# Performance work log

Measured on AMD Instinct MI355X. Metric: run time of the kernel, lower is better.

## Reference

```python
import jax, jax.numpy as jnp
import numpy as np

N_PROP, N_GRID, N_KEY, C_FEAT = 128, 216, 4096, 128
RADII = (0.8, 1.6)
NSAMPLES = (16, 16)
C_OUT = 64  # per-branch MLP output channels


def setup_inputs() -> dict:
    key = jax.random.key(0)
    ks = jax.random.split(key, 20)
    s = 0.05
    return {
        "wlh": jax.random.uniform(ks[0], (N_PROP, 3)) * 4.0 + 0.5,
        "center": jax.random.normal(ks[1], (N_PROP, 3)) * 5.0,
        "yaw": jax.random.uniform(ks[2], (N_PROP,)) * 2.0 * np.pi,
        "u": jax.random.uniform(ks[3], (N_PROP, N_GRID, 3)),
        "keypoints_xyz": jax.random.normal(ks[4], (1, N_KEY, 3)) * 5.0,
        "keypoints_features": jax.random.normal(ks[5], (1, C_FEAT, N_KEY)),
        "pn0_w1": jax.random.normal(ks[6], (C_OUT, C_FEAT + 3)) * s,
        "pn0_g1": jnp.ones((C_OUT,)), "pn0_b1": jnp.zeros((C_OUT,)),
        "pn0_w2": jax.random.normal(ks[7], (C_OUT, C_OUT)) * s,
        "pn0_g2": jnp.ones((C_OUT,)), "pn0_b2": jnp.zeros((C_OUT,)),
        "pn1_w1": jax.random.normal(ks[8], (C_OUT, C_FEAT + 3)) * s,
        "pn1_g1": jnp.ones((C_OUT,)), "pn1_b1": jnp.zeros((C_OUT,)),
        "pn1_w2": jax.random.normal(ks[9], (C_OUT, C_OUT)) * s,
        "pn1_g2": jnp.ones((C_OUT,)), "pn1_b2": jnp.zeros((C_OUT,)),
        "red_w1": jax.random.normal(ks[10], (256, N_GRID * 2 * C_OUT)) * 0.01,
        "red_b1": jnp.zeros((256,)),
        "red_w2": jax.random.normal(ks[11], (256, 256)) * s,
        "red_b2": jnp.zeros((256,)),
    }


def reference(wlh, center, yaw, u, keypoints_xyz, keypoints_features,
              pn0_w1, pn0_g1, pn0_b1, pn0_w2, pn0_g2, pn0_b2,
              pn1_w1, pn1_g1, pn1_b1, pn1_w2, pn1_g2, pn1_b2,
              red_w1, red_b1, red_w2, red_b2):
    n, m, _ = u.shape
    # --- sample gridpoints inside proposals and rotate by yaw around z ---
    gp = u * wlh[:, None, :]                                 # (n, m, 3)
    c, s = jnp.cos(yaw), jnp.sin(yaw)
    R = jnp.stack([c, -s, s, c], axis=-1).reshape(-1, 2, 2)   # (n, 2, 2)
    xy = jnp.einsum('njk,nmk->nmj', R, gp[..., :2])
    grid = jnp.concatenate([xy, gp[..., 2:]], -1) + center[:, None, :]
    grid = grid.reshape(-1, 3)                               # (G, 3), G = n*m

    kp = keypoints_xyz[0]                                    # (K, 3)
    kf = jnp.transpose(keypoints_features[0])                # (K, C)
    K = kp.shape[0]

    # squared distances (G, K) without materializing (G, K, 3)
    d2 = (jnp.sum(grid * grid, -1)[:, None]
          + jnp.sum(kp * kp, -1)[None, :]
          - 2.0 * grid @ kp.T)

    def ball_query(radius, nsample):
        # first `nsample` in-radius indices in original order; pad with first
        # hit; all-zeros if no point in radius (pointnet2 CUDA semantics).
        mask = d2 < radius * radius
        cand = jnp.where(mask, jnp.arange(K, dtype=jnp.int32), K)
        srt = jnp.sort(cand, axis=-1)[:, :nsample]           # (G, ns)
        first = srt[:, :1]
        return jnp.where(srt < K, srt, jnp.where(first < K, first, 0))

    def branch(radius, nsample, w1, g1, b1, w2, g2, b2):
        idx = ball_query(radius, nsample)                    # (G, ns)
        xyz = kp[idx] - grid[:, None, :]                     # (G, ns, 3)
        x = jnp.concatenate([xyz, kf[idx]], -1)              # (G, ns, 3+C)
        h = jax.nn.relu(jnp.einsum('gnc,oc->gno', x, w1) * g1 + b1)
        h = jax.nn.relu(jnp.einsum('gnc,oc->gno', h, w2) * g2 + b2)
        return jnp.max(h, axis=1)                            # (G, C_OUT)

    f0 = branch(RADII[0], NSAMPLES[0], pn0_w1, pn0_g1, pn0_b1, pn0_w2, pn0_g2, pn0_b2)
    f1 = branch(RADII[1], NSAMPLES[1], pn1_w1, pn1_g1, pn1_b1, pn1_w2, pn1_g2, pn1_b2)
    pooled = jnp.concatenate([f0, f1], -1)                   # (G, 2*C_OUT)
    Cp = pooled.shape[-1]

    # faithful replication of (1,C,n,m).permute(0,3,1,2).view(1,n,-1)
    t = pooled.reshape(n, m, Cp)                             # gridpoint order (n, m)
    red_in = jnp.transpose(t, (1, 2, 0)).reshape(1, n, m * Cp)

    h = jax.nn.relu(red_in @ red_w1.T + red_b1)
    return jax.nn.relu(h @ red_w2.T + red_b2)                # (1, n, 256)
```

## Files before the change

### kernel.cpp

```cpp
#include <hip/hip_runtime.h>
#include <hip/hip_bf16.h>

typedef unsigned short u16;
typedef unsigned int   u32;
typedef unsigned long long u64;

#define N_PROPC 128
#define N_GRIDC 216
#define G_TOT   27648
#define N_KEYC  4096
#define C_FEATC 128
#define R0SQ    0.64f
#define R1SQ    2.56f
#define BF16_ONES_DWORD 0x3F803F80u

typedef __attribute__((ext_vector_type(8))) short bf16x8;
typedef __attribute__((ext_vector_type(4))) float f32x4;

#if __has_builtin(__builtin_amdgcn_fcmpf)
#define BALLOT_LT(a, b) __builtin_amdgcn_fcmpf((a), (b), 4)
#else
#define BALLOT_LT(a, b) __ballot((a) < (b))
#endif

__device__ __forceinline__ float bf2f(u16 u) {
    return __uint_as_float(((u32)u) << 16);
}
__device__ __forceinline__ u16 f2bf(float f) {
    u32 u = __float_as_uint(f);
    u32 r = (u + 0x7fffu + ((u >> 16) & 1u)) >> 16;
    return (u16)r;
}
__device__ __forceinline__ bool is_bf16(const u32* flagp) {
    return *flagp == BF16_ONES_DWORD;
}
__device__ __forceinline__ float ld(const void* p, int i, bool bf) {
    return bf ? bf2f(((const u16*)p)[i]) : ((const float*)p)[i];
}
__device__ __forceinline__ u16 ldb(const void* p, int i, bool bf) {
    return bf ? ((const u16*)p)[i] : f2bf(((const float*)p)[i]);
}

__global__ __launch_bounds__(256) void prep_fused_kernel(
    const u32* __restrict__ flagp,
    const void* __restrict__ kxyz,
    const void* __restrict__ wlh, const void* __restrict__ center,
    const void* __restrict__ yaw, const void* __restrict__ uu,
    const void* __restrict__ kf,
    const void* __restrict__ w10, const void* __restrict__ g10, const void* __restrict__ b10,
    const void* __restrict__ w20, const void* __restrict__ g20, const void* __restrict__ b20,
    const void* __restrict__ w11, const void* __restrict__ g11, const void* __restrict__ b11,
    const void* __restrict__ w21, const void* __restrict__ g21, const void* __restrict__ b21,
    const void* __restrict__ rw2,
    float4* __restrict__ kp4, float4* __restrict__ grid4, u16* __restrict__ kfT,
    u16* __restrict__ w1mf, u16* __restrict__ w2mf,
    float* __restrict__ g1f, float* __restrict__ b1f,
    float* __restrict__ g2f, float* __restrict__ b2f,
    float* __restrict__ w2rT)
{
    __shared__ u16 tile[64][130];
    const bool bf = is_bf16(flagp);
    const int bid = blockIdx.x, tid = threadIdx.x;

    if (bid < 16) {
        int k = bid * 256 + tid;
        float x = ld(kxyz, k*3, bf), y = ld(kxyz, k*3+1, bf), z = ld(kxyz, k*3+2, bf);
        kp4[k] = make_float4(x, y, z, 0.0f);
    } else if (bid < 124) {
        int g = (bid - 16) * 256 + tid;
        int n = g / N_GRIDC;
        float ux = ld(uu, g*3, bf), uy = ld(uu, g*3+1, bf), uz = ld(uu, g*3+2, bf);
        float gpx = ux * ld(wlh, n*3, bf);
        float gpy = uy * ld(wlh, n*3+1, bf);
        float gpz = uz * ld(wlh, n*3+2, bf);
        float yv = ld(yaw, n, bf);
        float c = cosf(yv), sn = sinf(yv);
        float x = (c*gpx - sn*gpy) + ld(center, n*3, bf);
        float y = (sn*gpx + c*gpy) + ld(center, n*3+1, bf);
        float z = gpz + ld(center, n*3+2, bf);
        grid4[g] = make_float4(x, y, z, 0.0f);
    } else if (bid < 188) {
        const int key0 = (bid - 124) * 64;
        #pragma unroll 4
        for (int rep = 0; rep < 32; ++rep) {
            int t = rep*256 + tid;
            int feat = t >> 6;
            int klo = t & 63;
            tile[klo][feat] = ldb(kf, feat * N_KEYC + key0 + klo, bf);
        }
        __syncthreads();
        #pragma unroll 4
        for (int rep = 0; rep < 32; ++rep) {
            int t = rep*256 + tid;
            int klo = t >> 7;
            int feat = t & 127;
            kfT[(key0 + klo)*128 + feat] = tile[klo][feat];
        }
    } else if (bid < 190) {
        const int b = bid - 188;
        const void* w1 = b ? w11 : w10; const void* g1v = b ? g11 : g10;
        const void* w2 = b ? w21 : w20; const void* g2v = b ? g21 : g20;
        const void* b1v = b ? b11 : b10; const void* b2v = b ? b21 : b20;
        for (int f = tid; f < 10240; f += 256) {
            int j = f & 7, t1 = f >> 3;
            int n = t1 & 15, t2 = t1 >> 4;
            int quad = t2 & 3, t3 = t2 >> 2;
            int kt = t3 % 5, nt = t3 / 5;
            int k = kt*32 + quad*8 + j;
            int o = nt*16 + n;
            u16 v = 0;
            if (k < 128)      v = ldb(w1, o*131 + 3 + k, bf);
            else if (k < 131) v = ldb(w1, o*131 + (k - 128), bf);
            w1mf[b*10240 + f] = v;
        }
        for (int f = tid; f < 4096; f += 256) {
            int j = f & 7, t1 = f >> 3;
            int n = t1 & 15, t2 = t1 >> 4;
            int quad = t2 & 3, t3 = t2 >> 2;
            int kt = t3 & 1, nt = t3 >> 1;
            int k = kt*32 + quad*8 + j;
            int o = nt*16 + n;
            w2mf[b*4096 + f] = ldb(w2, o*64 + k, bf);
        }
        if (tid < 64) {
            g1f[b*64 + tid] = ld(g1v, tid, bf);
            b1f[b*64 + tid] = ld(b1v, tid, bf);
            g2f[b*64 + tid] = ld(g2v, tid, bf);
            b2f[b*64 + tid] = ld(b2v, tid, bf);
        }
    } else {
        int t = (bid - 190) * 256 + tid;
        int o = t & 255, c = t >> 8;
        w2rT[c*256 + o] = ld(rw2, o*256 + c, bf);
    }
}

__global__ __launch_bounds__(256) void ballquery_kernel(
    const float4* __restrict__ kp4,
    const float4* __restrict__ grid4, u16* __restrict__ idx01)
{
    __shared__ __attribute__((aligned(16))) float4 sk[2048];
    const int tid = threadIdx.x;
    const int lane = tid & 63;
    const int wid = tid >> 6;
    const int g0 = blockIdx.x * 16 + wid * 4;
    const float4 gra = grid4[g0];
    const float4 grb = grid4[g0 + 1];
    const float4 grc = grid4[g0 + 2];
    const float4 grd = grid4[g0 + 3];

    u64 m0[4] = {0, 0, 0, 0};
    u64 m1[4] = {0, 0, 0, 0};
    #pragma unroll 1
    for (int pass = 0; pass < 2; ++pass) {
        if (pass) __syncthreads();
        for (int t = tid; t < 2048; t += 256) sk[t] = kp4[pass*2048 + t];
        __syncthreads();
        #pragma unroll
        for (int it = 0; it < 32; ++it) {
            const float4 kv = sk[it*64 + lane];
            const int chunk = pass*32 + it;
            float dx, dy, dz, d;
            dx = kv.x - gra.x; dy = kv.y - gra.y; dz = kv.z - gra.z;
            d = fmaf(dx, dx, fmaf(dy, dy, dz * dz));
            const u64 a1 = BALLOT_LT(d, R1SQ); const u64 a0 = BALLOT_LT(d, R0SQ);
            dx = kv.x - grb.x; dy = kv.y - grb.y; dz = kv.z - grb.z;
            d = fmaf(dx, dx, fmaf(dy, dy, dz * dz));
            const u64 b1m = BALLOT_LT(d, R1SQ); const u64 b0m = BALLOT_LT(d, R0SQ);
            dx = kv.x - grc.x; dy = kv.y - grc.y; dz = kv.z - grc.z;
            d = fmaf(dx, dx, fmaf(dy, dy, dz * dz));
            const u64 c1m = BALLOT_LT(d, R1SQ); const u64 c0m = BALLOT_LT(d, R0SQ);
            dx = kv.x - grd.x; dy = kv.y - grd.y; dz = kv.z - grd.z;
            d = fmaf(dx, dx, fmaf(dy, dy, dz * dz));
            const u64 d1m = BALLOT_LT(d, R1SQ); const u64 d0m = BALLOT_LT(d, R0SQ);
            if (lane == chunk) {
                m1[0] = a1; m0[0] = a0;
                m1[1] = b1m; m0[1] = b0m;
                m1[2] = c1m; m0[2] = c0m;
                m1[3] = d1m; m0[3] = d0m;
            }
        }
    }

    #pragma unroll
    for (int gg = 0; gg < 4; ++gg) {
        const int g = g0 + gg;
        u16* o0 = idx01 + (size_t)g * 16;
        u16* o1 = idx01 + (size_t)G_TOT * 16 + (size_t)g * 16;
        #pragma unroll
        for (int rad = 0; rad < 2; ++rad) {
            u64 mask = rad ? m1[gg] : m0[gg];
            u16* op = rad ? o1 : o0;
            const int cnt = __popcll(mask);
            int inc = cnt;
            #pragma unroll
            for (int d = 1; d < 64; d <<= 1) {
                int t = __shfl_up(inc, d);
                if (lane >= d) inc += t;
            }
            const int pre = inc - cnt;
            int firstk = (cnt > 0 && pre == 0) ? (lane*64 + __ffsll(mask) - 1) : 0x7FFFFFFF;
            #pragma unroll
            for (int d = 32; d >= 1; d >>= 1)
                firstk = min(firstk, __shfl_xor(firstk, d));
            const int total = __shfl(inc, 63);
            u64 mrem = mask;
            int p = pre;
            while (mrem != 0 && p < 16) {
                int j = __ffsll(mrem) - 1;
                op[p] = (u16)(lane*64 + j);
                mrem &= mrem - 1;
                ++p;
            }
            if (lane < 16 && lane >= total)
                op[lane] = (u16)(firstk == 0x7FFFFFFF ? 0 : firstk);
        }
    }
}

__global__ __launch_bounds__(256) void pointnet_mfma_kernel(
    const float4* __restrict__ grid4, const float4* __restrict__ kp4,
    const u16* __restrict__ kfT,
    const u16* __restrict__ w1mf, const u16* __restrict__ w2mf,
    const float* __restrict__ g1f, const float* __restrict__ b1f,
    const float* __restrict__ g2f, const float* __restrict__ b2f,
    const u16* __restrict__ idx01, u16* __restrict__ ATb)
{
    __shared__ __attribute__((aligned(16))) u16 w1s[10240];
    __shared__ __attribute__((aligned(16))) u16 w2s[4096];
    __shared__ __attribute__((aligned(16))) u16 h1s[4][32*72];
    const int tid = threadIdx.x;
    const int branch = blockIdx.y;

    {
        const uint4* s1 = (const uint4*)(w1mf + branch*10240);
        uint4* d1 = (uint4*)w1s;
        for (int t = tid; t < 1280; t += 256) d1[t] = s1[t];
        const uint4* s2 = (const uint4*)(w2mf + branch*4096);
        uint4* d2 = (uint4*)w2s;
        for (int t = tid; t < 512; t += 256) d2[t] = s2[t];
    }
    __syncthreads();

    const int wid = tid >> 6, lane = tid & 63;
    const int n = lane & 15, quad = lane >> 4;
    const int mi = blockIdx.x % N_GRIDC;
    const int nig = blockIdx.x / N_GRIDC;
    const int ni0 = nig*16 + wid*4;

    float g1v[4], b1v[4], g2v[4], b2v[4];
    #pragma unroll
    for (int nt = 0; nt < 4; ++nt) {
        g1v[nt] = g1f[branch*64 + nt*16 + n];
        b1v[nt] = b1f[branch*64 + nt*16 + n];
        g2v[nt] = g2f[branch*64 + nt*16 + n];
        b2v[nt] = b2f[branch*64 + nt*16 + n];
    }

    int idxv[4];
    #pragma unroll
    for (int gg = 0; gg < 4; ++gg) {
        const int g = (ni0 + gg) * N_GRIDC + mi;
        idxv[gg] = idx01[(size_t)branch*(G_TOT*16) + g*16 + n] & (N_KEYC - 1);
    }

    u16* __restrict__ h1w = &h1s[wid][0];

    #pragma unroll 1
    for (int p = 0; p < 2; ++p) {
        const int niA = ni0 + 2*p, niB = niA + 1;
        const int idxA = idxv[2*p], idxB = idxv[2*p + 1];
        const float4 kpA = kp4[idxA];
        const float4 kpB = kp4[idxB];
        const float4 grA = grid4[niA * N_GRIDC + mi];
        const float4 grB = grid4[niB * N_GRIDC + mi];

        const u16* __restrict__ arowA = kfT + idxA * C_FEATC;
        const u16* __restrict__ arowB = kfT + idxB * C_FEATC;
        uint4 arA[4], arB[4];
        #pragma unroll
        for (int kt = 0; kt < 4; ++kt) {
            arA[kt] = *(const uint4*)(arowA + kt*32 + quad*8);
            arB[kt] = *(const uint4*)(arowB + kt*32 + quad*8);
        }

        bf16x8 axyzA = (bf16x8)(short)0, axyzB = (bf16x8)(short)0;
        if (quad == 0) {
            axyzA[0] = (short)f2bf(kpA.x - grA.x);
            axyzA[1] = (short)f2bf(kpA.y - grA.y);
            axyzA[2] = (short)f2bf(kpA.z - grA.z);
            axyzB[0] = (short)f2bf(kpB.x - grB.x);
            axyzB[1] = (short)f2bf(kpB.y - grB.y);
            axyzB[2] = (short)f2bf(kpB.z - grB.z);
        }

        f32x4 accA[4], accB[4];
        #pragma unroll
        for (int nt = 0; nt < 4; ++nt) {
            accA[nt] = (f32x4){0.f, 0.f, 0.f, 0.f};
            accB[nt] = (f32x4){0.f, 0.f, 0.f, 0.f};
        }

        #pragma unroll
        for (int kt = 0; kt < 4; ++kt) {
            bf16x8 aA, aB;
            __builtin_memcpy(&aA, &arA[kt], 16);
            __builtin_memcpy(&aB, &arB[kt], 16);
            #pragma unroll
            for (int nt = 0; nt < 4; ++nt) {
                bf16x8 b = *(const bf16x8*)&w1s[(((nt*5 + kt)*4 + quad)*16 + n)*8];
                accA[nt] = __builtin_amdgcn_mfma_f32_16x16x32_bf16(aA, b, accA[nt], 0, 0, 0);
                accB[nt] = __builtin_amdgcn_mfma_f32_16x16x32_bf16(aB, b, accB[nt], 0, 0, 0);
            }
        }
        #pragma unroll
        for (int nt = 0; nt < 4; ++nt) {
            bf16x8 b = *(const bf16x8*)&w1s[(((nt*5 + 4)*4 + quad)*16 + n)*8];
            accA[nt] = __builtin_amdgcn_mfma_f32_16x16x32_bf16(axyzA, b, accA[nt], 0, 0, 0);
            accB[nt] = __builtin_amdgcn_mfma_f32_16x16x32_bf16(axyzB, b, accB[nt], 0, 0, 0);
        }

        #pragma unroll
        for (int nt = 0; nt < 4; ++nt) {
            #pragma unroll
            for (int r = 0; r < 4; ++r) {
                float vA = fmaxf(fmaf(accA[nt][r], g1v[nt], b1v[nt]), 0.0f);
                float vB = fmaxf(fmaf(accB[nt][r], g1v[nt], b1v[nt]), 0.0f);
                h1w[(quad*4 + r)*72 + nt*16 + n] = f2bf(vA);
                h1w[(16 + quad*4 + r)*72 + nt*16 + n] = f2bf(vB);
            }
        }

        f32x4 cA[4], cB[4];
        #pragma unroll
        for (int nt = 0; nt < 4; ++nt) {
            cA[nt] = (f32x4){0.f, 0.f, 0.f, 0.f};
            cB[nt] = (f32x4){0.f, 0.f, 0.f, 0.f};
        }
        #pragma unroll
        for (int kt = 0; kt < 2; ++kt) {
            bf16x8 a2A = *(const bf16x8*)&h1w[n*72 + kt*32 + quad*8];
            bf16x8 a2B = *(const bf16x8*)&h1w[(16 + n)*72 + kt*32 + quad*8];
            #pragma unroll
            for (int nt = 0; nt < 4; ++nt) {
                bf16x8 b = *(const bf16x8*)&w2s[(((nt*2 + kt)*4 + quad)*16 + n)*8];
                cA[nt] = __builtin_amdgcn_mfma_f32_16x16x32_bf16(a2A, b, cA[nt], 0, 0, 0);
                cB[nt] = __builtin_amdgcn_mfma_f32_16x16x32_bf16(a2B, b, cB[nt], 0, 0, 0);
            }
        }

        #pragma unroll
        for (int nt = 0; nt < 4; ++nt) {
            float vA = fmaxf(fmaxf(fmaxf(fmaf(cA[nt][0], g2v[nt], b2v[nt]), 0.0f),
                                   fmaxf(fmaf(cA[nt][1], g2v[nt], b2v[nt]), 0.0f)),
                             fmaxf(fmaxf(fmaf(cA[nt][2], g2v[nt], b2v[nt]), 0.0f),
                                   fmaxf(fmaf(cA[nt][3], g2v[nt], b2v[nt]), 0.0f)));
            float vB = fmaxf(fmaxf(fmaxf(fmaf(cB[nt][0], g2v[nt], b2v[nt]), 0.0f),
                                   fmaxf(fmaf(cB[nt][1], g2v[nt], b2v[nt]), 0.0f)),
                             fmaxf(fmaxf(fmaf(cB[nt][2], g2v[nt], b2v[nt]), 0.0f),
                                   fmaxf(fmaf(cB[nt][3], g2v[nt], b2v[nt]), 0.0f)));
            vA = fmaxf(vA, __shfl_xor(vA, 16));
            vA = fmaxf(vA, __shfl_xor(vA, 32));
            vB = fmaxf(vB, __shfl_xor(vB, 16));
            vB = fmaxf(vB, __shfl_xor(vB, 32));
            if (lane < 16) {
                const int ci = branch*64 + nt*16 + n;
                ATb[mi*16384 + ci*128 + niA] = f2bf(vA);
                ATb[mi*16384 + ci*128 + niB] = f2bf(vB);
            }
        }
    }
}

__global__ __launch_bounds__(256) void red1_mfma_kernel(
    const u32* __restrict__ flagp,
    const u16* __restrict__ ATb, const void* __restrict__ rw1,
    float* __restrict__ part)
{
    const bool bf = is_bf16(flagp);
    const int tid = threadIdx.x;
    const int wid = tid >> 6, lane = tid & 63;
    const int b = blockIdx.x;
    const int kc = b & 15;
    const int nt = (b >> 4) & 15;
    const int mt = (b >> 8) * 4 + wid;
    const int n = lane & 15, quad = lane >> 4;
    const int o = nt*16 + n;

    const u16* __restrict__ arow = ATb + (size_t)(mt*16 + n) * 27648;

    f32x4 acc = {0.f, 0.f, 0.f, 0.f};
    if (bf) {
        const u16* __restrict__ brow = (const u16*)rw1 + (size_t)o * 27648;
        #pragma unroll 2
        for (int s = 0; s < 54; ++s) {
            const int kk = kc*54 + s;
            uint4 araw = *(const uint4*)(arow + kk*32 + quad*8);
            bf16x8 a;
            __builtin_memcpy(&a, &araw, 16);
            uint4 braw = *(const uint4*)(brow + kk*32 + quad*8);
            bf16x8 bb;
            __builtin_memcpy(&bb, &braw, 16);
            acc = __builtin_amdgcn_mfma_f32_16x16x32_bf16(a, bb, acc, 0, 0, 0);
        }
    } else {
        const float* __restrict__ brow = (const float*)rw1 + (size_t)o * 27648;
        #pragma unroll 2
        for (int s = 0; s < 54; ++s) {
            const int kk = kc*54 + s;
            uint4 araw = *(const uint4*)(arow + kk*32 + quad*8);
            bf16x8 a;
            __builtin_memcpy(&a, &araw, 16);
            const float4 f0 = *(const float4*)(brow + kk*32 + quad*8);
            const float4 f1 = *(const float4*)(brow + kk*32 + quad*8 + 4);
            bf16x8 bb;
            bb[0] = (short)f2bf(f0.x); bb[1] = (short)f2bf(f0.y);
            bb[2] = (short)f2bf(f0.z); bb[3] = (short)f2bf(f0.w);
            bb[4] = (short)f2bf(f1.x); bb[5] = (short)f2bf(f1.y);
            bb[6] = (short)f2bf(f1.z); bb[7] = (short)f2bf(f1.w);
            acc = __builtin_amdgcn_mfma_f32_16x16x32_bf16(a, bb, acc, 0, 0, 0);
        }
    }
    #pragma unroll
    for (int r = 0; r < 4; ++r) {
        const int i = mt*16 + quad*4 + r;
        part[kc*32768 + i*256 + nt*16 + n] = acc[r];
    }
}

__global__ __launch_bounds__(256) void tail_kernel(
    const u32* __restrict__ flagp,
    const float* __restrict__ part, const void* __restrict__ rb1,
    const float* __restrict__ w2rT, const void* __restrict__ rb2,
    void* __restrict__ outp)
{
    __shared__ float hs[256];
    const bool bf = is_bf16(flagp);
    const int o = threadIdx.x, i = blockIdx.x;
    float s = ld(rb1, o, bf);
    #pragma unroll
    for (int kc = 0; kc < 16; ++kc) s += part[kc*32768 + i*256 + o];
    hs[o] = fmaxf(s, 0.0f);
    __syncthreads();
    float s2 = ld(rb2, o, bf);
    #pragma unroll 8
    for (int c = 0; c < 256; ++c)
        s2 = fmaf(hs[c], w2rT[c*256 + o], s2);
    float v = fmaxf(s2, 0.0f);
    if (bf) ((u16*)outp)[i*256 + o] = f2bf(v);
    else    ((float*)outp)[i*256 + o] = v;
}


extern "C" void kernel_launch(void* const* d_in, const int* in_sizes, int n_in,
                              void* d_out, int out_size, void* d_ws, size_t ws_size,
                              hipStream_t stream) {
    const void* wlh    = d_in[0];
    const void* center = d_in[1];
    const void* yaw    = d_in[2];
    const void* uu     = d_in[3];
    const void* kxyz   = d_in[4];
    const void* kfeat  = d_in[5];
    const void* p0w1 = d_in[6];  const void* p0g1 = d_in[7];
    const void* p0b1 = d_in[8];  const void* p0w2 = d_in[9];
    const void* p0g2 = d_in[10]; const void* p0b2 = d_in[11];
    const void* p1w1 = d_in[12]; const void* p1g1 = d_in[13];
    const void* p1b1 = d_in[14]; const void* p1w2 = d_in[15];
    const void* p1g2 = d_in[16]; const void* p1b2 = d_in[17];
    const void* rw1 = d_in[18];
    const void* rb1 = d_in[19];
    const void* rw2 = d_in[20];
    const void* rb2 = d_in[21];
    const u32* flagp = (const u32*)d_in[7];

    char* w = (char*)d_ws;
    float4* kp4   = (float4*)(w + 65536);
    float4* grid4 = (float4*)(w + 131072);
    u16*    kfT   = (u16*)(w + 573440);
    u16*    w1mf  = (u16*)(w + 1622016);
    u16*    w2mf  = (u16*)(w + 1662976);
    float*  g1f   = (float*)(w + 1679360);
    float*  b1f   = (float*)(w + 1679872);
    float*  g2f   = (float*)(w + 1680384);
    float*  b2f   = (float*)(w + 1680896);
    float*  w2rT  = (float*)(w + 1721856);
    u16*    idx01 = (u16*)(w + 1984000);
    u16*    ATb   = (u16*)(w + 3754496);
    float*  part  = (float*)(w + 32066048);

    prep_fused_kernel<<<446, 256, 0, stream>>>(flagp,
        kxyz, wlh, center, yaw, uu, kfeat,
        p0w1, p0g1, p0b1, p0w2, p0g2, p0b2,
        p1w1, p1g1, p1b1, p1w2, p1g2, p1b2,
        rw2,
        kp4, grid4, kfT,
        w1mf, w2mf, g1f, b1f, g2f, b2f, w2rT);

    ballquery_kernel<<<G_TOT/16, 256, 0, stream>>>(kp4, grid4, idx01);

    dim3 pngrid(G_TOT/16, 2);
    pointnet_mfma_kernel<<<pngrid, 256, 0, stream>>>(grid4, kp4, kfT, w1mf, w2mf,
                                                     g1f, b1f, g2f, b2f, idx01, ATb);

    red1_mfma_kernel<<<512, 256, 0, stream>>>(flagp, ATb, rw1, part);
    tail_kernel<<<128, 256, 0, stream>>>(flagp, part, rb1, w2rT, rb2, d_out);
}
```

Baseline: 271.7 us.

## Pre-convert reduce weights to bf16 in prep, double split-K, serialize pointnet halves

Adds a prep stage that converts the large red_w1 matrix (256 x 27648) to packed bf16 in workspace, so the red1 GEMM always takes the bf16 path and drops its runtime flag branch. The red1 split-K factor goes from 16 to 32, doubling the block count, and tail_kernel sums 32 partial slices. In the pointnet kernel the two gridpoints of each pair are now processed one after the other, halving the h1 shared buffer and packing the two bf16 outputs into a single 32-bit store. For fp32 inputs the conversion reads the full fp32 weight once and writes a bf16 copy, which adds traffic and about 14k extra prep blocks, and the extra partial slices cost more writes and reads.

Result: faster. 260.9 us (-4.0%).

```diff
diff --git a/kernel.cpp b/kernel.cpp
--- a/kernel.cpp
+++ b/kernel.cpp
@@ -51,12 +51,12 @@
     const void* __restrict__ w20, const void* __restrict__ g20, const void* __restrict__ b20,
     const void* __restrict__ w11, const void* __restrict__ g11, const void* __restrict__ b11,
     const void* __restrict__ w21, const void* __restrict__ g21, const void* __restrict__ b21,
-    const void* __restrict__ rw2,
+    const void* __restrict__ rw2, const void* __restrict__ rw1,
     float4* __restrict__ kp4, float4* __restrict__ grid4, u16* __restrict__ kfT,
     u16* __restrict__ w1mf, u16* __restrict__ w2mf,
     float* __restrict__ g1f, float* __restrict__ b1f,
     float* __restrict__ g2f, float* __restrict__ b2f,
-    float* __restrict__ w2rT)
+    float* __restrict__ w2rT, u32* __restrict__ rw1bf)
 {
     __shared__ u16 tile[64][130];
     const bool bf = is_bf16(flagp);
@@ -128,10 +128,19 @@
             g2f[b*64 + tid] = ld(g2v, tid, bf);
             b2f[b*64 + tid] = ld(b2v, tid, bf);
         }
-    } else {
+    } else if (bid < 446) {
         int t = (bid - 190) * 256 + tid;
         int o = t & 255, c = t >> 8;
         w2rT[c*256 + o] = ld(rw2, o*256 + c, bf);
+    } else {
+        int t = (bid - 446) * 256 + tid;
+        if (bf) {
+            rw1bf[t] = ((const u32*)rw1)[t];
+        } else {
+            const float* s = (const float*)rw1;
+            u32 lo = f2bf(s[2*t]), hi = f2bf(s[2*t + 1]);
+            rw1bf[t] = lo | (hi << 16);
+        }
     }
 }
 
@@ -228,7 +237,7 @@
 {
     __shared__ __attribute__((aligned(16))) u16 w1s[10240];
     __shared__ __attribute__((aligned(16))) u16 w2s[4096];
-    __shared__ __attribute__((aligned(16))) u16 h1s[4][32*72];
+    __shared__ __attribute__((aligned(16))) u16 h1s[4][16*72];
     const int tid = threadIdx.x;
     const int branch = blockIdx.y;
 
@@ -268,12 +277,12 @@
 
     #pragma unroll 1
     for (int p = 0; p < 2; ++p) {
-        const int niA = ni0 + 2*p, niB = niA + 1;
+        const int niA = ni0 + 2*p;
         const int idxA = idxv[2*p], idxB = idxv[2*p + 1];
         const float4 kpA = kp4[idxA];
         const float4 kpB = kp4[idxB];
         const float4 grA = grid4[niA * N_GRIDC + mi];
-        const float4 grB = grid4[niB * N_GRIDC + mi];
+        const float4 grB = grid4[(niA + 1) * N_GRIDC + mi];
 
         const u16* __restrict__ arowA = kfT + idxA * C_FEATC;
         const u16* __restrict__ arowB = kfT + idxB * C_FEATC;
@@ -320,106 +329,80 @@
             accB[nt] = __builtin_amdgcn_mfma_f32_16x16x32_bf16(axyzB, b, accB[nt], 0, 0, 0);
         }
 
-        #pragma unroll
-        for (int nt = 0; nt < 4; ++nt) {
-            #pragma unroll
-            for (int r = 0; r < 4; ++r) {
-                float vA = fmaxf(fmaf(accA[nt][r], g1v[nt], b1v[nt]), 0.0f);
-                float vB = fmaxf(fmaf(accB[nt][r], g1v[nt], b1v[nt]), 0.0f);
-                h1w[(quad*4 + r)*72 + nt*16 + n] = f2bf(vA);
-                h1w[(16 + quad*4 + r)*72 + nt*16 + n] = f2bf(vB);
-            }
-        }
-
-        f32x4 cA[4], cB[4];
-        #pragma unroll
-        for (int nt = 0; nt < 4; ++nt) {
-            cA[nt] = (f32x4){0.f, 0.f, 0.f, 0.f};
-            cB[nt] = (f32x4){0.f, 0.f, 0.f, 0.f};
-        }
-        #pragma unroll
-        for (int kt = 0; kt < 2; ++kt) {
-            bf16x8 a2A = *(const bf16x8*)&h1w[n*72 + kt*32 + quad*8];
-            bf16x8 a2B = *(const bf16x8*)&h1w[(16 + n)*72 + kt*32 + quad*8];
+        float outv[2][4];
+        #pragma unroll
+        for (int ab = 0; ab < 2; ++ab) {
+            const f32x4* acc = ab ? accB : accA;
             #pragma unroll
             for (int nt = 0; nt < 4; ++nt) {
-                bf16x8 b = *(const bf16x8*)&w2s[(((nt*2 + kt)*4 + quad)*16 + n)*8];
-                cA[nt] = __builtin_amdgcn_mfma_f32_16x16x32_bf16(a2A, b, cA[nt], 0, 0, 0);
-                cB[nt] = __builtin_amdgcn_mfma_f32_16x16x32_bf16(a2B, b, cB[nt], 0, 0, 0);
-            }
-        }
-
-        #pragma unroll
-        for (int nt = 0; nt < 4; ++nt) {
-            float vA = fmaxf(fmaxf(fmaxf(fmaf(cA[nt][0], g2v[nt], b2v[nt]), 0.0f),
-                                   fmaxf(fmaf(cA[nt][1], g2v[nt], b2v[nt]), 0.0f)),
-                             fmaxf(fmaxf(fmaf(cA[nt][2], g2v[nt], b2v[nt]), 0.0f),
-                                   fmaxf(fmaf(cA[nt][3], g2v[nt], b2v[nt]), 0.0f)));
-            float vB = fmaxf(fmaxf(fmaxf(fmaf(cB[nt][0], g2v[nt], b2v[nt]), 0.0f),
-                                   fmaxf(fmaf(cB[nt][1], g2v[nt], b2v[nt]), 0.0f)),
-                             fmaxf(fmaxf(fmaf(cB[nt][2], g2v[nt], b2v[nt]), 0.0f),
-                                   fmaxf(fmaf(cB[nt][3], g2v[nt], b2v[nt]), 0.0f)));
-            vA = fmaxf(vA, __shfl_xor(vA, 16));
-            vA = fmaxf(vA, __shfl_xor(vA, 32));
-            vB = fmaxf(vB, __shfl_xor(vB, 16));
-            vB = fmaxf(vB, __shfl_xor(vB, 32));
-            if (lane < 16) {
+                #pragma unroll
+                for (int r = 0; r < 4; ++r) {
+                    float v = fmaxf(fmaf(acc[nt][r], g1v[nt], b1v[nt]), 0.0f);
+                    h1w[(quad*4 + r)*72 + nt*16 + n] = f2bf(v);
+                }
+            }
+            f32x4 c2[4];
+            #pragma unroll
+            for (int nt = 0; nt < 4; ++nt) c2[nt] = (f32x4){0.f, 0.f, 0.f, 0.f};
+            #pragma unroll
+            for (int kt = 0; kt < 2; ++kt) {
+                bf16x8 a2 = *(const bf16x8*)&h1w[n*72 + kt*32 + quad*8];
+                #pragma unroll
+                for (int nt = 0; nt < 4; ++nt) {
+                    bf16x8 b = *(const bf16x8*)&w2s[(((nt*2 + kt)*4 + quad)*16 + n)*8];
+                    c2[nt] = __builtin_amdgcn_mfma_f32_16x16x32_bf16(a2, b, c2[nt], 0, 0, 0);
+                }
+            }
+            #pragma unroll
+            for (int nt = 0; nt < 4; ++nt) {
+                float v = fmaxf(fmaxf(fmaxf(fmaf(c2[nt][0], g2v[nt], b2v[nt]), 0.0f),
+                                      fmaxf(fmaf(c2[nt][1], g2v[nt], b2v[nt]), 0.0f)),
+                                fmaxf(fmaxf(fmaf(c2[nt][2], g2v[nt], b2v[nt]), 0.0f),
+                                      fmaxf(fmaf(c2[nt][3], g2v[nt], b2v[nt]), 0.0f)));
+                v = fmaxf(v, __shfl_xor(v, 16));
+                v = fmaxf(v, __shfl_xor(v, 32));
+                outv[ab][nt] = v;
+            }
+        }
+
+        if (lane < 16) {
+            #pragma unroll
+            for (int nt = 0; nt < 4; ++nt) {
                 const int ci = branch*64 + nt*16 + n;
-                ATb[mi*16384 + ci*128 + niA] = f2bf(vA);
-                ATb[mi*16384 + ci*128 + niB] = f2bf(vB);
+                const u32 pk = (u32)f2bf(outv[0][nt]) | ((u32)f2bf(outv[1][nt]) << 16);
+                *(u32*)&ATb[mi*16384 + ci*128 + niA] = pk;
             }
         }
     }
 }
 
 __global__ __launch_bounds__(256) void red1_mfma_kernel(
-    const u32* __restrict__ flagp,
-    const u16* __restrict__ ATb, const void* __restrict__ rw1,
+    const u16* __restrict__ ATb, const u16* __restrict__ rw1bf,
     float* __restrict__ part)
 {
-    const bool bf = is_bf16(flagp);
     const int tid = threadIdx.x;
     const int wid = tid >> 6, lane = tid & 63;
     const int b = blockIdx.x;
-    const int kc = b & 15;
-    const int nt = (b >> 4) & 15;
-    const int mt = (b >> 8) * 4 + wid;
+    const int kc = b & 31;
+    const int nt = (b >> 5) & 15;
+    const int mt = (b >> 9) * 4 + wid;
     const int n = lane & 15, quad = lane >> 4;
     const int o = nt*16 + n;
 
     const u16* __restrict__ arow = ATb + (size_t)(mt*16 + n) * 27648;
+    const u16* __restrict__ brow = rw1bf + (size_t)o * 27648;
 
     f32x4 acc = {0.f, 0.f, 0.f, 0.f};
-    if (bf) {
-        const u16* __restrict__ brow = (const u16*)rw1 + (size_t)o * 27648;
-        #pragma unroll 2
-        for (int s = 0; s < 54; ++s) {
-            const int kk = kc*54 + s;
-            uint4 araw = *(const uint4*)(arow + kk*32 + quad*8);
-            bf16x8 a;
-            __builtin_memcpy(&a, &araw, 16);
-            uint4 braw = *(const uint4*)(brow + kk*32 + quad*8);
-            bf16x8 bb;
-            __builtin_memcpy(&bb, &braw, 16);
-            acc = __builtin_amdgcn_mfma_f32_16x16x32_bf16(a, bb, acc, 0, 0, 0);
-        }
-    } else {
-        const float* __restrict__ brow = (const float*)rw1 + (size_t)o * 27648;
-        #pragma unroll 2
-        for (int s = 0; s < 54; ++s) {
-            const int kk = kc*54 + s;
-            uint4 araw = *(const uint4*)(arow + kk*32 + quad*8);
-            bf16x8 a;
-            __builtin_memcpy(&a, &araw, 16);
-            const float4 f0 = *(const float4*)(brow + kk*32 + quad*8);
-            const float4 f1 = *(const float4*)(brow + kk*32 + quad*8 + 4);
-            bf16x8 bb;
-            bb[0] = (short)f2bf(f0.x); bb[1] = (short)f2bf(f0.y);
-            bb[2] = (short)f2bf(f0.z); bb[3] = (short)f2bf(f0.w);
-            bb[4] = (short)f2bf(f1.x); bb[5] = (short)f2bf(f1.y);
-            bb[6] = (short)f2bf(f1.z); bb[7] = (short)f2bf(f1.w);
-            acc = __builtin_amdgcn_mfma_f32_16x16x32_bf16(a, bb, acc, 0, 0, 0);
-        }
+    #pragma unroll 3
+    for (int s = 0; s < 27; ++s) {
+        const int kk = kc*27 + s;
+        uint4 araw = *(const uint4*)(arow + kk*32 + quad*8);
+        bf16x8 a;
+        __builtin_memcpy(&a, &araw, 16);
+        uint4 braw = *(const uint4*)(brow + kk*32 + quad*8);
+        bf16x8 bb;
+        __builtin_memcpy(&bb, &braw, 16);
+        acc = __builtin_amdgcn_mfma_f32_16x16x32_bf16(a, bb, acc, 0, 0, 0);
     }
     #pragma unroll
     for (int r = 0; r < 4; ++r) {
@@ -439,7 +422,7 @@
     const int o = threadIdx.x, i = blockIdx.x;
     float s = ld(rb1, o, bf);
     #pragma unroll
-    for (int kc = 0; kc < 16; ++kc) s += part[kc*32768 + i*256 + o];
+    for (int kc = 0; kc < 32; ++kc) s += part[kc*32768 + i*256 + o];
     hs[o] = fmaxf(s, 0.0f);
     __syncthreads();
     float s2 = ld(rb2, o, bf);
@@ -486,15 +469,16 @@
     float*  w2rT  = (float*)(w + 1721856);
     u16*    idx01 = (u16*)(w + 1984000);
     u16*    ATb   = (u16*)(w + 3754496);
+    u32*    rw1bf = (u32*)(w + 17910272);
     float*  part  = (float*)(w + 32066048);
 
-    prep_fused_kernel<<<446, 256, 0, stream>>>(flagp,
+    prep_fused_kernel<<<14270, 256, 0, stream>>>(flagp,
         kxyz, wlh, center, yaw, uu, kfeat,
         p0w1, p0g1, p0b1, p0w2, p0g2, p0b2,
         p1w1, p1g1, p1b1, p1w2, p1g2, p1b2,
-        rw2,
+        rw2, rw1,
         kp4, grid4, kfT,
-        w1mf, w2mf, g1f, b1f, g2f, b2f, w2rT);
+        w1mf, w2mf, g1f, b1f, g2f, b2f, w2rT, rw1bf);
 
     ballquery_kernel<<<G_TOT/16, 256, 0, stream>>>(kp4, grid4, idx01);
 
@@ -502,6 +486,6 @@
     pointnet_mfma_kernel<<<pngrid, 256, 0, stream>>>(grid4, kp4, kfT, w1mf, w2mf,
                                                      g1f, b1f, g2f, b2f, idx01, ATb);
 
-    red1_mfma_kernel<<<512, 256, 0, stream>>>(flagp, ATb, rw1, part);
+    red1_mfma_kernel<<<1024, 256, 0, stream>>>(ATb, (const u16*)rw1bf, part);
     tail_kernel<<<128, 256, 0, stream>>>(flagp, part, rb1, w2rT, rb2, d_out);
 }
```
